# Performance work log

Measured on AMD Instinct MI355X. Metric: run time of the kernel, lower is better.

The kernel has to match this reference:

```python
import jax, jax.numpy as jnp
import numpy as np

B, S, D, H = 2, 2048, 2048, 16
HD = D // H  # head_dim = 128


def setup_inputs() -> dict:
    key = jax.random.key(0)
    ks = jax.random.split(key, 7)
    s = 0.02
    return {
        "q": jax.random.normal(ks[0], (B, S, D), jnp.float32),
        "k": jax.random.normal(ks[1], (B, S, D), jnp.float32),
        "v": jax.random.normal(ks[2], (B, S, D), jnp.float32),
        "wq": jax.random.normal(ks[3], (D, D), jnp.float32) * s,
        "wk": jax.random.normal(ks[4], (D, D), jnp.float32) * s,
        "wv": jax.random.normal(ks[5], (D, D), jnp.float32) * s,
        "wo": jax.random.normal(ks[6], (D, D), jnp.float32) * s,
    }


def reference(q, k, v, wq, wk, wv, wo):
    # Linear(bias=False): y = x @ W.T  (torch weight layout [out, in])
    xq = jnp.einsum("bse,me->bsm", q, wq).reshape(B, S, H, HD).transpose(0, 2, 1, 3)
    xk = jnp.einsum("bse,me->bsm", k, wk).reshape(B, S, H, HD).transpose(0, 2, 1, 3)
    xv = jnp.einsum("bse,me->bsm", v, wv).reshape(B, S, H, HD).transpose(0, 2, 1, 3)
    scores = jnp.einsum("bhqd,bhkd->bhqk", xq, xk) / jnp.sqrt(jnp.float32(HD))
    # causal mask: -inf above diagonal
    causal = jnp.tril(jnp.ones((S, S), dtype=bool))
    scores = jnp.where(causal[None, None], scores, jnp.float32(-jnp.inf))
    probs = jax.nn.softmax(scores.astype(jnp.float32), axis=-1)
    out = jnp.einsum("bhqk,bhkd->bhqd", probs, xv)  # [B,H,S,HD]
    out = out.transpose(0, 2, 1, 3).reshape(B, S, D)
    out = jnp.einsum("bsm,em->bse", out, wo)
    return out
```

## Files before the change

kernel.cpp:

```cpp
#include <hip/hip_runtime.h>

typedef __bf16 bf16x8 __attribute__((ext_vector_type(8)));
typedef float f32x4 __attribute__((ext_vector_type(4)));

__device__ inline unsigned short f2bf(float f) {
  unsigned int u = __float_as_uint(f);
  u = (u + 0x7FFFu + ((u >> 16) & 1u)) >> 16;
  return (unsigned short)u;
}

__device__ inline void gl_lds16(const void* g, void* l) {
  __builtin_amdgcn_global_load_lds(
      (__attribute__((address_space(1))) const void*)g,
      (__attribute__((address_space(3))) void*)l, 16, 0, 0);
}

__global__ __launch_bounds__(256) void zero_f4(float* __restrict__ p, int n4) {
  int i = blockIdx.x * 256 + threadIdx.x;
  if (i < n4) ((float4*)p)[i] = make_float4(0.f, 0.f, 0.f, 0.f);
}

__global__ __launch_bounds__(256) void cvt_batch(const float* __restrict__ p0,
                                                 const float* __restrict__ p1,
                                                 const float* __restrict__ p2,
                                                 const float* __restrict__ p3,
                                                 unsigned short* __restrict__ out,
                                                 int n4each) {
  const int y = blockIdx.y;
  const float* src = (y == 0) ? p0 : (y == 1) ? p1 : (y == 2) ? p2 : p3;
  unsigned short* dst = out + (size_t)y * n4each * 4;
  int i = blockIdx.x * 256 + threadIdx.x;
  if (i >= n4each) return;
  const float4 v = ((const float4*)src)[i];
  ushort4 o;
  o.x = f2bf(v.x); o.y = f2bf(v.y); o.z = f2bf(v.z); o.w = f2bf(v.w);
  ((ushort4*)dst)[i] = o;
}

template <int MODE>
__global__ __launch_bounds__(512, 2) void gemm8(const unsigned short* __restrict__ A,
                                                const unsigned short* __restrict__ Wb,
                                                void* __restrict__ Cv,
                                                int N, int Kloop, int lda,
                                                float qscale) {
  extern __shared__ char lds[];
  const int tid = threadIdx.x;
  const int w = tid >> 6, l = tid & 63;
  const int wr = w >> 2, wc = w & 3;

  const int nbx = N >> 8;
  const int cpx = gridDim.x >> 3;
  const int bid = blockIdx.x;
  const int swz = (bid & 7) * cpx + (bid >> 3);
  const int by = swz / nbx, bx = swz % nbx;
  const int m0 = by << 8, n0 = bx << 8;

  const unsigned short* W = Wb;
  const unsigned short* Ab = A;
  float scale = 1.0f;
  int seg = 0;
  if (MODE == 0) {
    seg = m0 >> 12;
    W = Wb + (size_t)seg * 2048 * 2048;
    scale = (seg == 0) ? qscale : 1.0f;
  } else {
    const int koff = blockIdx.y * Kloop;
    Ab = A + koff;
    W = Wb + koff;
  }

  const int col_l = ((l & 3) * 8) ^ ((l >= 32) ? 16 : 0);
  const size_t rowA0 = (size_t)(m0 + w * 16 + (l >> 2)) * lda + col_l;
  const size_t rowA1 = rowA0 + (size_t)128 * lda;
  const size_t rowB0 = (size_t)(n0 + w * 16 + (l >> 2)) * lda + col_l;
  const size_t rowB1 = rowB0 + (size_t)128 * lda;
  const int stA = w * 2048;

  const int Sread = ((l & 15) * 64 + (l >> 4) * 16) ^ ((l & 8) << 2);
  const int ldsAr = wr * 16384 + Sread;
  const int ldsBr = 32768 + (wc >> 1) * 16384 + Sread;

  const f32x4 fz = {0.f, 0.f, 0.f, 0.f};
  f32x4 acc[8][4];
#pragma unroll
  for (int i = 0; i < 8; i++)
#pragma unroll
    for (int j = 0; j < 4; j++) acc[i][j] = fz;
  bf16x8 af[2][4], bfr[2][4];

#define STAGE_A(b, h, kb)                                                           \
  gl_lds16(Ab + ((h) ? rowA1 : rowA0) + (kb), lds + (b) * 65536 + (h) * 16384 + stA); \
  gl_lds16(Ab + ((h) ? rowA1 : rowA0) + (kb) + 32,                                  \
           lds + (b) * 65536 + (h) * 16384 + stA + 1024)

#define STAGE_B(b, h, kb)                                                  \
  gl_lds16(W + ((h) ? rowB1 : rowB0) + (kb),                               \
           lds + (b) * 65536 + 32768 + (h) * 16384 + stA);                 \
  gl_lds16(W + ((h) ? rowB1 : rowB0) + (kb) + 32,                          \
           lds + (b) * 65536 + 32768 + (h) * 16384 + stA + 1024)

#define LDA(b, qi)                                                                   \
  _Pragma("unroll") for (int i = 0; i < 4; ++i) {                                    \
    af[0][i] = *(const bf16x8*)(lds + (b) * 65536 + ldsAr + ((qi) * 4 + i) * 2048);  \
    af[1][i] =                                                                       \
        *(const bf16x8*)(lds + (b) * 65536 + ldsAr + ((qi) * 4 + i) * 2048 + 1024);  \
  }

#define LDB(b, qj)                                                                    \
  _Pragma("unroll") for (int j = 0; j < 2; ++j) {                                     \
    bfr[0][(qj) * 2 + j] = *(const bf16x8*)(lds + (b) * 65536 + ldsBr +               \
                                            ((wc & 1) * 4 + (qj) * 2 + j) * 2048);    \
    bfr[1][(qj) * 2 + j] = *(const bf16x8*)(lds + (b) * 65536 + ldsBr +               \
                                            ((wc & 1) * 4 + (qj) * 2 + j) * 2048 +    \
                                            1024);                                    \
  }

#define MM(qi, qj)                                                              \
  __builtin_amdgcn_s_setprio(1);                                                \
  _Pragma("unroll") for (int ks = 0; ks < 2; ++ks)                              \
      _Pragma("unroll") for (int i = 0; i < 4; ++i)                             \
          _Pragma("unroll") for (int j = 0; j < 2; ++j) acc[(qi) * 4 + i]       \
                                                           [(qj) * 2 + j] =     \
      __builtin_amdgcn_mfma_f32_16x16x32_bf16(                                  \
          af[ks][i], bfr[ks][(qj) * 2 + j], acc[(qi) * 4 + i][(qj) * 2 + j], 0, \
          0, 0);                                                                \
  __builtin_amdgcn_s_setprio(0)

#define BAR                      \
  __builtin_amdgcn_s_barrier(); \
  __builtin_amdgcn_sched_barrier(0)
#define WL0                                          \
  asm volatile("s_waitcnt lgkmcnt(0)" ::: "memory"); \
  __builtin_amdgcn_sched_barrier(0)
#define WV4                                         \
  asm volatile("s_waitcnt vmcnt(4)" ::: "memory"); \
  __builtin_amdgcn_sched_barrier(0)

  STAGE_A(0, 0, 0);
  STAGE_A(0, 1, 0);
  STAGE_B(0, 0, 0);
  STAGE_B(0, 1, 0);
  STAGE_B(1, 0, 64);
  STAGE_B(1, 1, 64);
  WV4;
  BAR;

  const int NT = Kloop >> 6;
  const int NI = NT >> 1;
  for (int it = 0; it < NI; ++it) {
    const int t1k = (2 * it + 1) * 64;
    const int t2k = ((2 * it + 2) < NT ? (2 * it + 2) : 0) * 64;
    const int t3k = ((2 * it + 3) < NT ? (2 * it + 3) : 1) * 64;

    LDA(0, 0);
    LDB(0, 0);
    STAGE_A(1, 0, t1k);
    BAR; WL0;
    MM(0, 0);
    BAR;
    LDB(0, 1);
    STAGE_A(1, 1, t1k);
    BAR; WL0;
    MM(0, 1);
    BAR;
    LDA(0, 1);
    STAGE_B(0, 0, t2k);
    BAR; WL0;
    MM(1, 1);
    BAR;
    STAGE_B(0, 1, t2k);
    BAR;
    MM(1, 0);
    WV4;
    BAR;
    LDA(1, 0);
    LDB(1, 0);
    STAGE_A(0, 0, t2k);
    BAR; WL0;
    MM(0, 0);
    BAR;
    LDB(1, 1);
    STAGE_A(0, 1, t2k);
    BAR; WL0;
    MM(0, 1);
    BAR;
    LDA(1, 1);
    STAGE_B(1, 0, t3k);
    BAR; WL0;
    MM(1, 1);
    BAR;
    STAGE_B(1, 1, t3k);
    BAR;
    MM(1, 0);
    WV4;
    BAR;
  }
  asm volatile("s_waitcnt vmcnt(0)" ::: "memory");
  __builtin_amdgcn_sched_barrier(0);

  const int erow = m0 + wr * 128 + (l >> 4) * 4;
  const int ecol = n0 + wc * 64 + (l & 15);
  if (MODE == 0) {
    unsigned short* C = (unsigned short*)Cv;
    if (seg == 2) {
      const int b = (m0 - 8192) >> 11;
      const int s0 = ((m0 - 8192) & 2047) + wr * 128 + ((l >> 4) << 2);
      unsigned short* VT = C + (size_t)2 * 4096 * 2048;
#pragma unroll
      for (int i = 0; i < 8; i++)
#pragma unroll
        for (int j = 0; j < 4; j++) {
          const int c = ecol + j * 16;
          ushort4 o;
          o.x = f2bf(acc[i][j][0]); o.y = f2bf(acc[i][j][1]);
          o.z = f2bf(acc[i][j][2]); o.w = f2bf(acc[i][j][3]);
          *(ushort4*)&VT[((size_t)((b << 4) + (c >> 7)) * 128 + (c & 127)) * 2048 +
                         s0 + i * 16] = o;
        }
    } else {
#pragma unroll
      for (int i = 0; i < 8; i++)
#pragma unroll
        for (int j = 0; j < 4; j++)
#pragma unroll
          for (int r = 0; r < 4; r++)
            C[(size_t)(erow + i * 16 + r) * N + ecol + j * 16] =
                f2bf(acc[i][j][r] * scale);
    }
  } else {
    float* C = (float*)Cv;
#pragma unroll
    for (int i = 0; i < 8; i++)
#pragma unroll
      for (int j = 0; j < 4; j++)
#pragma unroll
        for (int r = 0; r < 4; r++)
          atomicAdd(&C[(size_t)(erow + i * 16 + r) * N + ecol + j * 16],
                    acc[i][j][r]);
  }
#undef STAGE_A
#undef STAGE_B
#undef LDA
#undef LDB
#undef MM
#undef BAR
#undef WL0
#undef WV4
}

__global__ __launch_bounds__(256) void flash_attn(const unsigned short* __restrict__ Qb,
                                                  const unsigned short* __restrict__ Kb,
                                                  const unsigned short* __restrict__ Vt,
                                                  unsigned short* __restrict__ Ob) {
  extern __shared__ char flds[];
  const int h = blockIdx.x, b = blockIdx.y;
  const int tile = 31 - blockIdx.z;
  const int q0 = tile * 64;
  const int tid = threadIdx.x;
  const int w = tid >> 6, l = tid & 63;
  const int lm = l & 15, lk = l >> 4;

  bf16x8 qf[4];
  {
    const unsigned short* qr = Qb + (size_t)(b * 2048 + q0 + w * 16 + lm) * 2048 + h * 128;
    for (int dc = 0; dc < 4; dc++) qf[dc] = *(const bf16x8*)&qr[dc * 32 + lk * 8];
  }

  const f32x4 fz = {0.f, 0.f, 0.f, 0.f};
  float l_r[4] = {0.f, 0.f, 0.f, 0.f};
  f32x4 oacc[8];
  for (int jd = 0; jd < 8; jd++) oacc[jd] = fz;

  const int nkt = tile + 1;
  unsigned short* Pw = (unsigned short*)(flds + 65536) + w * 1024;

#define FSTAGE(kti, bi)                                                              \
  do {                                                                               \
    const int kt_ = (kti)*64;                                                        \
    unsigned short* kls = (unsigned short*)(flds + (bi)*16384);                      \
    unsigned short* vls = (unsigned short*)(flds + 32768 + (bi)*16384);              \
    for (int iss = 0; iss < 4; iss++)                                                \
      gl_lds16(Kb + (size_t)(b * 2048 + kt_ + w * 16 + lm) * 2048 + h * 128 +        \
                   (iss * 4 + lk) * 8,                                               \
               kls + (w * 16 + iss * 4) * 128);                                      \
    for (int t = 0; t < 2; t++) {                                                    \
      int dg = w * 2 + t;                                                            \
      for (int c = 0; c < 2; c++)                                                    \
        gl_lds16(Vt + (size_t)((b * 16 + h) * 128 + dg * 16 + lm) * 2048 + kt_ +     \
                     (c * 4 + lk) * 8,                                               \
                 vls + (dg * 8 + c * 4) * 128);                                      \
    }                                                                                \
  } while (0)

#define FBAR                     \
  __builtin_amdgcn_s_barrier(); \
  __builtin_amdgcn_sched_barrier(0)

  FSTAGE(0, 0);
  if (nkt > 1) FSTAGE(1, 1);
  asm volatile("s_waitcnt vmcnt(0)" ::: "memory");
  __builtin_amdgcn_sched_barrier(0);
  FBAR;

  for (int kti = 0; kti < nkt; kti++) {
    const int cur = kti & 1;
    const int kt = kti * 64;
    const unsigned short* lsKc = (const unsigned short*)(flds + cur * 16384);
    const unsigned short* lsVc = (const unsigned short*)(flds + 32768 + cur * 16384);

    f32x4 s[4];
    for (int jn = 0; jn < 4; jn++) s[jn] = fz;
    __builtin_amdgcn_s_setprio(1);
    for (int jn = 0; jn < 4; jn++)
      for (int dc = 0; dc < 4; dc++) {
        bf16x8 kf = *(const bf16x8*)&lsKc[(jn * 16 + dc * 4) * 128 + l * 8];
        s[jn] = __builtin_amdgcn_mfma_f32_16x16x32_bf16(qf[dc], kf, s[jn], 0, 0, 0);
      }
    __builtin_amdgcn_s_setprio(0);

    const int diag = (kt == q0);
    for (int jn = 0; jn < 4; jn++) {
      int kcol = kt + jn * 16 + lm;
      for (int r = 0; r < 4; r++) {
        int qrow = q0 + w * 16 + lk * 4 + r;
        float p = (diag && kcol > qrow) ? 0.0f : __expf(s[jn][r]);
        s[jn][r] = p;
        l_r[r] += p;
      }
    }

    for (int jn = 0; jn < 4; jn++)
      for (int r = 0; r < 4; r++)
        Pw[(jn * 2 + (lm >> 3)) * 128 + (lk * 4 + r) * 8 + (lm & 7)] = f2bf(s[jn][r]);

    __builtin_amdgcn_s_setprio(1);
    for (int c = 0; c < 2; c++) {
      bf16x8 pf = *(const bf16x8*)&Pw[c * 512 + l * 8];
      for (int jd = 0; jd < 8; jd++) {
        bf16x8 vf = *(const bf16x8*)&lsVc[(jd * 8 + c * 4) * 128 + l * 8];
        oacc[jd] = __builtin_amdgcn_mfma_f32_16x16x32_bf16(pf, vf, oacc[jd], 0, 0, 0);
      }
    }
    __builtin_amdgcn_s_setprio(0);

    FBAR;
    if (kti + 2 < nkt) {
      FSTAGE(kti + 2, cur);
      asm volatile("s_waitcnt vmcnt(8)" ::: "memory");
    } else {
      asm volatile("s_waitcnt vmcnt(0)" ::: "memory");
    }
    __builtin_amdgcn_sched_barrier(0);
    FBAR;
  }

  for (int r = 0; r < 4; r++)
    for (int off = 1; off < 16; off <<= 1) l_r[r] += __shfl_xor(l_r[r], off, 64);

  for (int jd = 0; jd < 8; jd++) {
    int dcol = h * 128 + jd * 16 + lm;
    for (int r = 0; r < 4; r++) {
      size_t idx = (size_t)(b * 2048 + q0 + w * 16 + lk * 4 + r) * 2048 + dcol;
      Ob[idx] = f2bf(oacc[jd][r] / l_r[r]);
    }
  }
#undef FSTAGE
#undef FBAR
}

extern "C" void kernel_launch(void* const* d_in, const int* in_sizes, int n_in,
                              void* d_out, int out_size, void* d_ws, size_t ws_size,
                              hipStream_t stream) {
  const float* q  = (const float*)d_in[0];
  const float* k  = (const float*)d_in[1];
  const float* v  = (const float*)d_in[2];
  const float* wq = (const float*)d_in[3];
  const float* wk = (const float*)d_in[4];
  const float* wv = (const float*)d_in[5];
  const float* wo = (const float*)d_in[6];
  float* out = (float*)d_out;

  static bool attr_done = false;
  if (!attr_done) {
    hipFuncSetAttribute((const void*)gemm8<0>,
                        hipFuncAttributeMaxDynamicSharedMemorySize, 131072);
    hipFuncSetAttribute((const void*)gemm8<1>,
                        hipFuncAttributeMaxDynamicSharedMemorySize, 131072);
    hipFuncSetAttribute((const void*)flash_attn,
                        hipFuncAttributeMaxDynamicSharedMemorySize, 73728);
    attr_done = true;
  }

  const size_t SD = (size_t)4096 * 2048;
  const size_t DD = (size_t)2048 * 2048;
  unsigned short* ws  = (unsigned short*)d_ws;
  unsigned short* qb  = ws;
  unsigned short* wqb = qb + 3 * SD;
  unsigned short* wob = wqb + 3 * DD;
  unsigned short* Qb  = wqb + 4 * DD;
  unsigned short* Kb  = Qb + SD;
  unsigned short* VT  = Kb + SD;
  unsigned short* Ob  = qb + SD;

  zero_f4<<<8192, 256, 0, stream>>>(out, (int)((size_t)4096 * 2048 / 4));

  cvt_batch<<<dim3(8192, 3), 256, 0, stream>>>(q, k, v, q, qb, (int)(SD / 4));
  cvt_batch<<<dim3(4096, 4), 256, 0, stream>>>(wq, wk, wv, wo, wqb, (int)(DD / 4));

  gemm8<0><<<dim3(384), 512, 131072, stream>>>(qb, wqb, (void*)Qb, 2048, 2048,
                                               2048, 0.08838834764831845f);

  flash_attn<<<dim3(16, 2, 32), 256, 73728, stream>>>(Qb, Kb, VT, Ob);

  gemm8<1><<<dim3(128, 2), 512, 131072, stream>>>(Ob, wob, (void*)out, 2048,
                                                  1024, 2048, 1.0f);
}
```

Baseline: 474.0 us.

## Shrink GEMM tile to 128x256 and drop split-K atomics for output projection

```diff
diff --git a/kernel.cpp b/kernel.cpp
--- a/kernel.cpp
+++ b/kernel.cpp
@@ -13,11 +13,6 @@
   __builtin_amdgcn_global_load_lds(
       (__attribute__((address_space(1))) const void*)g,
       (__attribute__((address_space(3))) void*)l, 16, 0, 0);
-}
-
-__global__ __launch_bounds__(256) void zero_f4(float* __restrict__ p, int n4) {
-  int i = blockIdx.x * 256 + threadIdx.x;
-  if (i < n4) ((float4*)p)[i] = make_float4(0.f, 0.f, 0.f, 0.f);
 }
 
 __global__ __launch_bounds__(256) void cvt_batch(const float* __restrict__ p0,
@@ -53,7 +48,7 @@
   const int bid = blockIdx.x;
   const int swz = (bid & 7) * cpx + (bid >> 3);
   const int by = swz / nbx, bx = swz % nbx;
-  const int m0 = by << 8, n0 = bx << 8;
+  const int m0 = by << 7, n0 = bx << 8;
 
   const unsigned short* W = Wb;
   const unsigned short* Ab = A;
@@ -63,67 +58,64 @@
     seg = m0 >> 12;
     W = Wb + (size_t)seg * 2048 * 2048;
     scale = (seg == 0) ? qscale : 1.0f;
-  } else {
-    const int koff = blockIdx.y * Kloop;
-    Ab = A + koff;
-    W = Wb + koff;
   }
 
   const int col_l = ((l & 3) * 8) ^ ((l >= 32) ? 16 : 0);
   const size_t rowA0 = (size_t)(m0 + w * 16 + (l >> 2)) * lda + col_l;
-  const size_t rowA1 = rowA0 + (size_t)128 * lda;
   const size_t rowB0 = (size_t)(n0 + w * 16 + (l >> 2)) * lda + col_l;
   const size_t rowB1 = rowB0 + (size_t)128 * lda;
   const int stA = w * 2048;
 
   const int Sread = ((l & 15) * 64 + (l >> 4) * 16) ^ ((l & 8) << 2);
-  const int ldsAr = wr * 16384 + Sread;
-  const int ldsBr = 32768 + (wc >> 1) * 16384 + Sread;
+  const int ldsAr = Sread;
+  const int ldsBr = 16384 + (wc >> 1) * 16384 + Sread;
 
   const f32x4 fz = {0.f, 0.f, 0.f, 0.f};
-  f32x4 acc[8][4];
-#pragma unroll
-  for (int i = 0; i < 8; i++)
+  f32x4 acc[4][4];
+#pragma unroll
+  for (int i = 0; i < 4; i++)
 #pragma unroll
     for (int j = 0; j < 4; j++) acc[i][j] = fz;
-  bf16x8 af[2][4], bfr[2][4];
-
-#define STAGE_A(b, h, kb)                                                           \
-  gl_lds16(Ab + ((h) ? rowA1 : rowA0) + (kb), lds + (b) * 65536 + (h) * 16384 + stA); \
-  gl_lds16(Ab + ((h) ? rowA1 : rowA0) + (kb) + 32,                                  \
-           lds + (b) * 65536 + (h) * 16384 + stA + 1024)
-
-#define STAGE_B(b, h, kb)                                                  \
-  gl_lds16(W + ((h) ? rowB1 : rowB0) + (kb),                               \
-           lds + (b) * 65536 + 32768 + (h) * 16384 + stA);                 \
-  gl_lds16(W + ((h) ? rowB1 : rowB0) + (kb) + 32,                          \
-           lds + (b) * 65536 + 32768 + (h) * 16384 + stA + 1024)
-
-#define LDA(b, qi)                                                                   \
-  _Pragma("unroll") for (int i = 0; i < 4; ++i) {                                    \
-    af[0][i] = *(const bf16x8*)(lds + (b) * 65536 + ldsAr + ((qi) * 4 + i) * 2048);  \
-    af[1][i] =                                                                       \
-        *(const bf16x8*)(lds + (b) * 65536 + ldsAr + ((qi) * 4 + i) * 2048 + 1024);  \
-  }
-
-#define LDB(b, qj)                                                                    \
-  _Pragma("unroll") for (int j = 0; j < 2; ++j) {                                     \
-    bfr[0][(qj) * 2 + j] = *(const bf16x8*)(lds + (b) * 65536 + ldsBr +               \
-                                            ((wc & 1) * 4 + (qj) * 2 + j) * 2048);    \
-    bfr[1][(qj) * 2 + j] = *(const bf16x8*)(lds + (b) * 65536 + ldsBr +               \
-                                            ((wc & 1) * 4 + (qj) * 2 + j) * 2048 +    \
-                                            1024);                                    \
-  }
-
-#define MM(qi, qj)                                                              \
-  __builtin_amdgcn_s_setprio(1);                                                \
-  _Pragma("unroll") for (int ks = 0; ks < 2; ++ks)                              \
-      _Pragma("unroll") for (int i = 0; i < 4; ++i)                             \
-          _Pragma("unroll") for (int j = 0; j < 2; ++j) acc[(qi) * 4 + i]       \
-                                                           [(qj) * 2 + j] =     \
-      __builtin_amdgcn_mfma_f32_16x16x32_bf16(                                  \
-          af[ks][i], bfr[ks][(qj) * 2 + j], acc[(qi) * 4 + i][(qj) * 2 + j], 0, \
-          0, 0);                                                                \
+  bf16x8 af[2][2], bfr[2][4];
+
+#define STAGE_A(b, kb)                                        \
+  gl_lds16(Ab + rowA0 + (kb), lds + (b) * 49152 + stA);       \
+  gl_lds16(Ab + rowA0 + (kb) + 32, lds + (b) * 49152 + stA + 1024)
+
+#define STAGE_B(b, h, kb)                                                 \
+  gl_lds16(W + ((h) ? rowB1 : rowB0) + (kb),                              \
+           lds + (b) * 49152 + 16384 + (h) * 16384 + stA);                \
+  gl_lds16(W + ((h) ? rowB1 : rowB0) + (kb) + 32,                         \
+           lds + (b) * 49152 + 16384 + (h) * 16384 + stA + 1024)
+
+#define LDA(b, qi)                                                             \
+  _Pragma("unroll") for (int i = 0; i < 2; ++i) {                              \
+    af[0][i] = *(const bf16x8*)(lds + (b) * 49152 + ldsAr +                    \
+                                (wr * 4 + (qi) * 2 + i) * 2048);               \
+    af[1][i] = *(const bf16x8*)(lds + (b) * 49152 + ldsAr +                    \
+                                (wr * 4 + (qi) * 2 + i) * 2048 + 1024);        \
+  }
+
+#define LDB(b, qj)                                                             \
+  _Pragma("unroll") for (int j = 0; j < 2; ++j) {                              \
+    bfr[0][(qj) * 2 + j] = *(const bf16x8*)(lds + (b) * 49152 + ldsBr +        \
+                                            ((wc & 1) * 4 + (qj) * 2 + j) *    \
+                                                2048);                         \
+    bfr[1][(qj) * 2 + j] = *(const bf16x8*)(lds + (b) * 49152 + ldsBr +        \
+                                            ((wc & 1) * 4 + (qj) * 2 + j) *    \
+                                                2048 +                         \
+                                            1024);                             \
+  }
+
+#define MM(qi, qj)                                                             \
+  __builtin_amdgcn_s_setprio(1);                                               \
+  _Pragma("unroll") for (int ks = 0; ks < 2; ++ks)                             \
+      _Pragma("unroll") for (int i = 0; i < 2; ++i)                            \
+          _Pragma("unroll") for (int j = 0; j < 2; ++j)                        \
+              acc[(qi) * 2 + i][(qj) * 2 + j] =                                \
+      __builtin_amdgcn_mfma_f32_16x16x32_bf16(af[ks][i], bfr[ks][(qj) * 2 + j],\
+                                              acc[(qi) * 2 + i][(qj) * 2 + j], \
+                                              0, 0, 0);                        \
   __builtin_amdgcn_s_setprio(0)
 
 #define BAR                      \
@@ -136,8 +128,7 @@
   asm volatile("s_waitcnt vmcnt(4)" ::: "memory"); \
   __builtin_amdgcn_sched_barrier(0)
 
-  STAGE_A(0, 0, 0);
-  STAGE_A(0, 1, 0);
+  STAGE_A(0, 0);
   STAGE_B(0, 0, 0);
   STAGE_B(0, 1, 0);
   STAGE_B(1, 0, 64);
@@ -154,12 +145,11 @@
 
     LDA(0, 0);
     LDB(0, 0);
-    STAGE_A(1, 0, t1k);
+    STAGE_A(1, t1k);
     BAR; WL0;
     MM(0, 0);
     BAR;
     LDB(0, 1);
-    STAGE_A(1, 1, t1k);
     BAR; WL0;
     MM(0, 1);
     BAR;
@@ -175,12 +165,11 @@
     BAR;
     LDA(1, 0);
     LDB(1, 0);
-    STAGE_A(0, 0, t2k);
+    STAGE_A(0, t2k);
     BAR; WL0;
     MM(0, 0);
     BAR;
     LDB(1, 1);
-    STAGE_A(0, 1, t2k);
     BAR; WL0;
     MM(0, 1);
     BAR;
@@ -198,16 +187,16 @@
   asm volatile("s_waitcnt vmcnt(0)" ::: "memory");
   __builtin_amdgcn_sched_barrier(0);
 
-  const int erow = m0 + wr * 128 + (l >> 4) * 4;
+  const int erow = m0 + wr * 64 + (l >> 4) * 4;
   const int ecol = n0 + wc * 64 + (l & 15);
   if (MODE == 0) {
     unsigned short* C = (unsigned short*)Cv;
     if (seg == 2) {
       const int b = (m0 - 8192) >> 11;
-      const int s0 = ((m0 - 8192) & 2047) + wr * 128 + ((l >> 4) << 2);
+      const int s0 = ((m0 - 8192) & 2047) + wr * 64 + ((l >> 4) << 2);
       unsigned short* VT = C + (size_t)2 * 4096 * 2048;
 #pragma unroll
-      for (int i = 0; i < 8; i++)
+      for (int i = 0; i < 4; i++)
 #pragma unroll
         for (int j = 0; j < 4; j++) {
           const int c = ecol + j * 16;
@@ -219,7 +208,7 @@
         }
     } else {
 #pragma unroll
-      for (int i = 0; i < 8; i++)
+      for (int i = 0; i < 4; i++)
 #pragma unroll
         for (int j = 0; j < 4; j++)
 #pragma unroll
@@ -230,13 +219,12 @@
   } else {
     float* C = (float*)Cv;
 #pragma unroll
-    for (int i = 0; i < 8; i++)
+    for (int i = 0; i < 4; i++)
 #pragma unroll
       for (int j = 0; j < 4; j++)
 #pragma unroll
         for (int r = 0; r < 4; r++)
-          atomicAdd(&C[(size_t)(erow + i * 16 + r) * N + ecol + j * 16],
-                    acc[i][j][r]);
+          C[(size_t)(erow + i * 16 + r) * N + ecol + j * 16] = acc[i][j][r];
   }
 #undef STAGE_A
 #undef STAGE_B
@@ -383,9 +371,9 @@
   static bool attr_done = false;
   if (!attr_done) {
     hipFuncSetAttribute((const void*)gemm8<0>,
-                        hipFuncAttributeMaxDynamicSharedMemorySize, 131072);
+                        hipFuncAttributeMaxDynamicSharedMemorySize, 98304);
     hipFuncSetAttribute((const void*)gemm8<1>,
-                        hipFuncAttributeMaxDynamicSharedMemorySize, 131072);
+                        hipFuncAttributeMaxDynamicSharedMemorySize, 98304);
     hipFuncSetAttribute((const void*)flash_attn,
                         hipFuncAttributeMaxDynamicSharedMemorySize, 73728);
     attr_done = true;
@@ -402,16 +390,14 @@
   unsigned short* VT  = Kb + SD;
   unsigned short* Ob  = qb + SD;
 
-  zero_f4<<<8192, 256, 0, stream>>>(out, (int)((size_t)4096 * 2048 / 4));
-
   cvt_batch<<<dim3(8192, 3), 256, 0, stream>>>(q, k, v, q, qb, (int)(SD / 4));
   cvt_batch<<<dim3(4096, 4), 256, 0, stream>>>(wq, wk, wv, wo, wqb, (int)(DD / 4));
 
-  gemm8<0><<<dim3(384), 512, 131072, stream>>>(qb, wqb, (void*)Qb, 2048, 2048,
-                                               2048, 0.08838834764831845f);
+  gemm8<0><<<dim3(768), 512, 98304, stream>>>(qb, wqb, (void*)Qb, 2048, 2048,
+                                              2048, 0.08838834764831845f);
 
   flash_attn<<<dim3(16, 2, 32), 256, 73728, stream>>>(Qb, Kb, VT, Ob);
 
-  gemm8<1><<<dim3(128, 2), 512, 131072, stream>>>(Ob, wob, (void*)out, 2048,
-                                                  1024, 2048, 1.0f);
-}
+  gemm8<1><<<dim3(256), 512, 98304, stream>>>(Ob, wob, (void*)out, 2048, 2048,
+                                              2048, 1.0f);
+}
```

New measurement: 410.0 us. 1.16x faster.
